# Performance work log

Hardware: AMD Instinct MI355X
Metric: run time of the kernel (lower is better)

The kernel has to match this reference:

```python
import jax, jax.numpy as jnp
import numpy as np

S, D, P, R, E, M, K = 1024, 1024, 2816, 64, 8, 16, 1


def setup_inputs() -> dict:
    key = jax.random.key(0)
    ks = jax.random.split(key, 10)
    xav_a = (2.0 / (P + R)) ** 0.5   # xavier_uniform-like std for adapters
    xav_d = (2.0 / (D + P)) ** 0.5   # xavier for down projections
    bank_s = (1.0 / D) ** 0.5        # keep basis columns O(1)
    return {
        "hidden_states": jax.random.normal(ks[0], (S, D), jnp.float32),
        "expert_indices": jax.random.randint(ks[1], (S, K), 0, E),
        "expert_weights": jax.random.uniform(ks[2], (S, K), jnp.float32),
        "up_adapters": jax.random.normal(ks[3], (E, P, R), jnp.float32) * xav_a,
        "gate_adapters": jax.random.normal(ks[4], (E, P, R), jnp.float32) * xav_a,
        "up_mixture_logits": jax.random.normal(ks[5], (E, M), jnp.float32) * 0.01,
        "gate_mixture_logits": jax.random.normal(ks[6], (E, M), jnp.float32) * 0.01,
        "down_projections": jax.random.normal(ks[7], (E, D, P), jnp.float32) * xav_d,
        "up_bank": jax.random.normal(ks[8], (M, D, R), jnp.float32) * bank_s,
        "gate_bank": jax.random.normal(ks[9], (M, D, R), jnp.float32) * bank_s,
    }


def reference(hidden_states, expert_indices, expert_weights,
              up_adapters, gate_adapters, up_mixture_logits,
              gate_mixture_logits, down_projections, up_bank, gate_bank):
    n_experts = down_projections.shape[0]
    # SparseMixer: token-independent mixture weights over global bases (softmax)
    alpha_up = jax.nn.softmax(up_mixture_logits, axis=-1)      # [E, M]
    alpha_gate = jax.nn.softmax(gate_mixture_logits, axis=-1)  # [E, M]
    # Compose per-expert mixed bases: sum_j alpha_{e,j} B_j -> [E, D, R]
    up_mixed = jnp.einsum('em,mdr->edr', alpha_up, up_bank)
    gate_mixed = jnp.einsum('em,mdr->edr', alpha_gate, gate_bank)
    # Recomposed Up/Gate weights: A_e @ mixed_e^T -> [E, P, D]
    W_up = jnp.einsum('epr,edr->epd', up_adapters, up_mixed)
    W_gate = jnp.einsum('epr,edr->epd', gate_adapters, gate_mixed)
    # Combine routing weights per (token, expert): sum over topk slots
    onehot = (expert_indices[..., None] == jnp.arange(n_experts)).astype(hidden_states.dtype)  # [S,K,E]
    comb = jnp.einsum('ske,sk->se', onehot, expert_weights)  # [S, E]
    out = jnp.zeros_like(hidden_states)
    for e in range(n_experts):  # fixed small expert count
        up = hidden_states @ W_up[e].T        # [S, P]
        gate = hidden_states @ W_gate[e].T    # [S, P]
        inter = jax.nn.silu(gate) * up        # gated activation
        out = out + (inter @ down_projections[e].T) * comb[:, e:e + 1]
    return out
```

## Files before the change

### kernel.cpp

```cpp
#include <hip/hip_runtime.h>
#include <hip/hip_bf16.h>
#include <math.h>

#define S 1024
#define D 1024
#define P 2816
#define R 64
#define E 8
#define M 16
#define KSPLIT 4
#define KQ (P / KSPLIT)
#define NIT (KQ / 64)
#define ZT 16
#define ACH ((E * P * R) / 8)

typedef __attribute__((ext_vector_type(8))) short short8;
typedef __attribute__((ext_vector_type(4))) float floatx4;

static __device__ inline unsigned short f2bf(float f) {
  __hip_bfloat16 h = __float2bfloat16(f);
  return *reinterpret_cast<unsigned short*>(&h);
}
static __device__ inline short8 pack8(float4 a, float4 b) {
  short8 v;
  v[0] = f2bf(a.x); v[1] = f2bf(a.y); v[2] = f2bf(a.z); v[3] = f2bf(a.w);
  v[4] = f2bf(b.x); v[5] = f2bf(b.y); v[6] = f2bf(b.z); v[7] = f2bf(b.w);
  return v;
}

__global__ __launch_bounds__(256) void k_pre(
    const float* __restrict__ H, const float* __restrict__ Aup,
    const float* __restrict__ Agate, const int* __restrict__ idx,
    unsigned short* __restrict__ Hbf, unsigned short* __restrict__ Aubf,
    unsigned short* __restrict__ Agbf, int* __restrict__ perm,
    int* __restrict__ offs) {
  int b = blockIdx.x, t = threadIdx.x;
  int g = b * 256 + t;

  if (b == 0) {
    __shared__ int hist[E];
    __shared__ int basearr[E];
    if (t < E) hist[t] = 0;
    __syncthreads();
    int e4[4];
#pragma unroll
    for (int j = 0; j < 4; ++j) {
      e4[j] = idx[t + j * 256];
      atomicAdd(&hist[e4[j]], 1);
    }
    __syncthreads();
    if (t == 0) {
      int run = 0;
      for (int i = 0; i < E; ++i) { basearr[i] = run; offs[i] = run; run += hist[i]; }
      offs[E] = S;
    }
    __syncthreads();
#pragma unroll
    for (int j = 0; j < 4; ++j) {
      int pos = atomicAdd(&basearr[e4[j]], 1);
      perm[pos] = t + j * 256;
    }
  }

  {
    const float* hs = H + (size_t)g * 16;
    float4 h0 = *(const float4*)hs, h1 = *(const float4*)(hs + 4);
    float4 h2 = *(const float4*)(hs + 8), h3 = *(const float4*)(hs + 12);
    *(short8*)(Hbf + (size_t)g * 16) = pack8(h0, h1);
    *(short8*)(Hbf + (size_t)g * 16 + 8) = pack8(h2, h3);
  }
#pragma unroll
  for (int j = 0; j < 3; ++j) {
    int c = g + j * 65536;
    if (c < ACH) {
      const float* su = Aup + (size_t)c * 8;
      const float* sg = Agate + (size_t)c * 8;
      float4 u0 = *(const float4*)su, u1 = *(const float4*)(su + 4);
      float4 g0 = *(const float4*)sg, g1 = *(const float4*)(sg + 4);
      *(short8*)(Aubf + (size_t)c * 8) = pack8(u0, u1);
      *(short8*)(Agbf + (size_t)c * 8) = pack8(g0, g1);
    }
  }
}

__global__ __launch_bounds__(256) void k_mix(
    const float* __restrict__ up_logits, const float* __restrict__ gate_logits,
    const float* __restrict__ up_bank, const float* __restrict__ gate_bank,
    unsigned short* __restrict__ mxT) {
  int mat = blockIdx.x;
  int d0 = blockIdx.y * 16;
  const float* bank = mat ? gate_bank : up_bank;
  __shared__ float alpha[E][M];
  __shared__ float tile[E][64][17];
  int t = threadIdx.x;
  if (t < E) {
    const float* lg = (mat ? gate_logits : up_logits) + t * M;
    float v[M], mx = -1e30f, s = 0.f;
#pragma unroll
    for (int m = 0; m < M; ++m) { v[m] = lg[m]; mx = fmaxf(mx, v[m]); }
#pragma unroll
    for (int m = 0; m < M; ++m) { v[m] = expf(v[m] - mx); s += v[m]; }
#pragma unroll
    for (int m = 0; m < M; ++m) alpha[t][m] = v[m] / s;
  }
  __syncthreads();
  int r4 = (t & 15) * 4;
  int dg = t >> 4;
  float val[E][4];
#pragma unroll
  for (int e = 0; e < E; ++e)
#pragma unroll
    for (int i = 0; i < 4; ++i) val[e][i] = 0.f;
  for (int m = 0; m < M; ++m) {
    float4 bv = *(const float4*)(bank + ((size_t)m * D + d0 + dg) * R + r4);
#pragma unroll
    for (int e = 0; e < E; ++e) {
      float a = alpha[e][m];
      val[e][0] += a * bv.x; val[e][1] += a * bv.y;
      val[e][2] += a * bv.z; val[e][3] += a * bv.w;
    }
  }
#pragma unroll
  for (int e = 0; e < E; ++e)
#pragma unroll
    for (int i = 0; i < 4; ++i) tile[e][r4 + i][dg] = val[e][i];
  __syncthreads();
  int e = t >> 5;
#pragma unroll
  for (int half = 0; half < 2; ++half) {
    int rr = (t & 31) + half * 32;
    short8 o0, o1;
#pragma unroll
    for (int j = 0; j < 8; ++j) {
      o0[j] = (short)f2bf(tile[e][rr][j]);
      o1[j] = (short)f2bf(tile[e][rr][8 + j]);
    }
    unsigned short* dst = mxT + ((size_t)(e * 128 + mat * 64 + rr)) * D + d0;
    *(short8*)dst = o0;
    *(short8*)(dst + 8) = o1;
  }
}

__global__ __launch_bounds__(64) void k_t(
    const unsigned short* __restrict__ Hbf, const unsigned short* __restrict__ mxT,
    const int* __restrict__ perm, const int* __restrict__ offs,
    float* __restrict__ tpart) {
  int e = blockIdx.x;
  int end = offs[e + 1];
  int row0 = offs[e] + blockIdx.y * 16;
  if (row0 >= end) return;
  int lane = threadIdx.x & 63;
  int quad = lane >> 4, l15 = lane & 15;
  int z = blockIdx.z;
  int k0 = z * (D / ZT);
  int pos = row0 + l15;
  int tok = (pos < end) ? perm[pos] : -1;
  const unsigned short* hrow = Hbf + (size_t)(tok < 0 ? 0 : tok) * D + k0;
  const unsigned short* brow = mxT + (size_t)e * 128 * D + k0;
  floatx4 acc[8];
#pragma unroll
  for (int nt = 0; nt < 8; ++nt) acc[nt] = (floatx4){0.f, 0.f, 0.f, 0.f};
#pragma unroll
  for (int ks = 0; ks < 2; ++ks) {
    int kc = ks * 32 + quad * 8;
    short8 a = (short8){0, 0, 0, 0, 0, 0, 0, 0};
    if (tok >= 0) a = *(const short8*)(hrow + kc);
#pragma unroll
    for (int nt = 0; nt < 8; ++nt) {
      short8 bb = *(const short8*)(brow + (size_t)(nt * 16 + l15) * D + kc);
      acc[nt] = __builtin_amdgcn_mfma_f32_16x16x32_bf16(a, bb, acc[nt], 0, 0, 0);
    }
  }
#pragma unroll
  for (int reg = 0; reg < 4; ++reg) {
    int p = row0 + quad * 4 + reg;
    if (p < end) {
#pragma unroll
      for (int nt = 0; nt < 8; ++nt)
        tpart[((size_t)z * S + p) * 128 + nt * 16 + l15] = acc[nt][reg];
    }
  }
}

__global__ __launch_bounds__(256) void k_tred(
    const float* __restrict__ tpart, unsigned short* __restrict__ tbuf) {
  int i = (blockIdx.x * 256 + threadIdx.x) * 2;
  float2 s = make_float2(0.f, 0.f);
#pragma unroll
  for (int z = 0; z < ZT; ++z) {
    float2 v = *(const float2*)(tpart + (size_t)z * S * 128 + i);
    s.x += v.x; s.y += v.y;
  }
  unsigned int pk = (unsigned int)f2bf(s.x) | ((unsigned int)f2bf(s.y) << 16);
  *(unsigned int*)(tbuf + i) = pk;
}

__global__ __launch_bounds__(256) void k_inter(
    const unsigned short* __restrict__ tbuf, const unsigned short* __restrict__ Aubf,
    const unsigned short* __restrict__ Agbf, const int* __restrict__ offs,
    unsigned short* __restrict__ inter) {
  int e = blockIdx.x;
  int start = offs[e] + blockIdx.y * 16;
  int end = offs[e + 1];
  if (start >= end) return;
  int t = threadIdx.x, lane = t & 63, w = t >> 6;
  int quad = lane >> 4, l15 = lane & 15;
  int p0 = blockIdx.z * 256 + w * 64;
  int pos = start + l15;
  bool okA = pos < end;
  floatx4 accu[4], accg[4];
#pragma unroll
  for (int nt = 0; nt < 4; ++nt) {
    accu[nt] = (floatx4){0.f, 0.f, 0.f, 0.f};
    accg[nt] = (floatx4){0.f, 0.f, 0.f, 0.f};
  }
#pragma unroll
  for (int ks = 0; ks < 2; ++ks) {
    int kc = ks * 32 + quad * 8;
    short8 au = (short8){0, 0, 0, 0, 0, 0, 0, 0};
    short8 ag = (short8){0, 0, 0, 0, 0, 0, 0, 0};
    if (okA) {
      au = *(const short8*)(tbuf + (size_t)pos * 128 + kc);
      ag = *(const short8*)(tbuf + (size_t)pos * 128 + 64 + kc);
    }
#pragma unroll
    for (int nt = 0; nt < 4; ++nt) {
      size_t prow = (size_t)e * P + p0 + nt * 16 + l15;
      short8 bu = *(const short8*)(Aubf + prow * R + kc);
      short8 bg = *(const short8*)(Agbf + prow * R + kc);
      accu[nt] = __builtin_amdgcn_mfma_f32_16x16x32_bf16(au, bu, accu[nt], 0, 0, 0);
      accg[nt] = __builtin_amdgcn_mfma_f32_16x16x32_bf16(ag, bg, accg[nt], 0, 0, 0);
    }
  }
#pragma unroll
  for (int nt = 0; nt < 4; ++nt)
#pragma unroll
    for (int reg = 0; reg < 4; ++reg) {
      int prow = start + quad * 4 + reg;
      if (prow < end) {
        float gv = accg[nt][reg], uv = accu[nt][reg];
        float val = uv * (gv / (1.f + __expf(-gv)));
        inter[(size_t)prow * P + p0 + nt * 16 + l15] = f2bf(val);
      }
    }
}

__global__ __launch_bounds__(256) void k_down(
    const unsigned short* __restrict__ inter, const float* __restrict__ Wd,
    const int* __restrict__ offs, float* __restrict__ dpart) {
  int e = blockIdx.x;
  int start = offs[e];
  int end = offs[e + 1];
  if (start >= end) return;
  int kz = blockIdx.y;
  int d0 = blockIdx.z * 64;
  __shared__ unsigned short As[256][72];
  __shared__ unsigned short Bs[64][72];
  int t = threadIdx.x;
  int lane = t & 63, w = t >> 6, quad = lane >> 4, l15 = lane & 15;

  const unsigned short* aptr[8];
  bool aok[8];
#pragma unroll
  for (int j = 0; j < 8; ++j) {
    int arow = (t >> 3) + 32 * j;
    int pos = start + arow;
    aok[j] = (pos < end);
    aptr[j] = inter + (size_t)(aok[j] ? pos : start) * P + kz * KQ + (t & 7) * 8;
  }
  const float* bsrc = Wd + ((size_t)(e * D + d0 + (t >> 2)) * P + kz * KQ + (t & 3) * 16);

  float4 pa[8];
  float4 pb[4];
#pragma unroll
  for (int j = 0; j < 8; ++j)
    pa[j] = aok[j] ? *(const float4*)(aptr[j]) : make_float4(0.f, 0.f, 0.f, 0.f);
#pragma unroll
  for (int q = 0; q < 4; ++q) pb[q] = *(const float4*)(bsrc + q * 4);

  floatx4 acc[4][4];
#pragma unroll
  for (int tt = 0; tt < 4; ++tt)
#pragma unroll
    for (int dt = 0; dt < 4; ++dt) acc[tt][dt] = (floatx4){0.f, 0.f, 0.f, 0.f};

  for (int it = 0; it < NIT; ++it) {
#pragma unroll
    for (int j = 0; j < 8; ++j)
      *(float4*)&As[(t >> 3) + 32 * j][(t & 7) * 8] = pa[j];
    {
      short8 bv0, bv1;
      bv0[0] = f2bf(pb[0].x); bv0[1] = f2bf(pb[0].y); bv0[2] = f2bf(pb[0].z); bv0[3] = f2bf(pb[0].w);
      bv0[4] = f2bf(pb[1].x); bv0[5] = f2bf(pb[1].y); bv0[6] = f2bf(pb[1].z); bv0[7] = f2bf(pb[1].w);
      bv1[0] = f2bf(pb[2].x); bv1[1] = f2bf(pb[2].y); bv1[2] = f2bf(pb[2].z); bv1[3] = f2bf(pb[2].w);
      bv1[4] = f2bf(pb[3].x); bv1[5] = f2bf(pb[3].y); bv1[6] = f2bf(pb[3].z); bv1[7] = f2bf(pb[3].w);
      *(short8*)&Bs[t >> 2][(t & 3) * 16] = bv0;
      *(short8*)&Bs[t >> 2][(t & 3) * 16 + 8] = bv1;
    }
    __syncthreads();
    if (it + 1 < NIT) {
      int k0 = (it + 1) * 64;
#pragma unroll
      for (int j = 0; j < 8; ++j)
        pa[j] = aok[j] ? *(const float4*)(aptr[j] + k0) : make_float4(0.f, 0.f, 0.f, 0.f);
#pragma unroll
      for (int q = 0; q < 4; ++q) pb[q] = *(const float4*)(bsrc + k0 + q * 4);
    }
#pragma unroll
    for (int ks = 0; ks < 2; ++ks) {
      int kc = ks * 32 + quad * 8;
      short8 a[4], b[4];
#pragma unroll
      for (int tt = 0; tt < 4; ++tt) a[tt] = *(const short8*)&As[w * 64 + tt * 16 + l15][kc];
#pragma unroll
      for (int dt = 0; dt < 4; ++dt) b[dt] = *(const short8*)&Bs[dt * 16 + l15][kc];
#pragma unroll
      for (int tt = 0; tt < 4; ++tt)
#pragma unroll
        for (int dt = 0; dt < 4; ++dt)
          acc[tt][dt] = __builtin_amdgcn_mfma_f32_16x16x32_bf16(a[tt], b[dt], acc[tt][dt], 0, 0, 0);
    }
    __syncthreads();
  }
  float* dp = dpart + (size_t)kz * S * D;
#pragma unroll
  for (int tt = 0; tt < 4; ++tt)
#pragma unroll
    for (int reg = 0; reg < 4; ++reg) {
      int pos = start + w * 64 + tt * 16 + quad * 4 + reg;
      if (pos < end) {
#pragma unroll
        for (int dt = 0; dt < 4; ++dt)
          dp[(size_t)pos * D + d0 + dt * 16 + l15] = acc[tt][dt][reg];
      }
    }
}

__global__ __launch_bounds__(256) void k_red(
    const float* __restrict__ dpart, const int* __restrict__ perm,
    const float* __restrict__ wts, float* __restrict__ out) {
  int t = threadIdx.x;
  int row = blockIdx.x * 4 + (t >> 6);
  int lane = t & 63;
  int tok = perm[row];
  float wt = wts[tok];
  const float* src = dpart + (size_t)row * D + lane * 4;
  float* dst = out + (size_t)tok * D + lane * 4;
#pragma unroll
  for (int j = 0; j < 4; ++j) {
    float4 s = *(const float4*)(src + j * 256);
#pragma unroll
    for (int kz = 1; kz < KSPLIT; ++kz) {
      float4 v = *(const float4*)(src + (size_t)kz * S * D + j * 256);
      s.x += v.x; s.y += v.y; s.z += v.z; s.w += v.w;
    }
    s.x *= wt; s.y *= wt; s.z *= wt; s.w *= wt;
    *(float4*)(dst + j * 256) = s;
  }
}

extern "C" void kernel_launch(void* const* d_in, const int* in_sizes, int n_in,
                              void* d_out, int out_size, void* d_ws, size_t ws_size,
                              hipStream_t stream) {
  const float* H = (const float*)d_in[0];
  const int* idx = (const int*)d_in[1];
  const float* wts = (const float*)d_in[2];
  const float* Aup = (const float*)d_in[3];
  const float* Agate = (const float*)d_in[4];
  const float* upl = (const float*)d_in[5];
  const float* gatel = (const float*)d_in[6];
  const float* Wd = (const float*)d_in[7];
  const float* upb = (const float*)d_in[8];
  const float* gateb = (const float*)d_in[9];
  float* out = (float*)d_out;

  char* ws = (char*)d_ws;
  unsigned short* Hbf = (unsigned short*)ws;
  unsigned short* mxT = Hbf + (size_t)S * D;
  unsigned short* Aubf = mxT + (size_t)E * 128 * D;
  unsigned short* Agbf = Aubf + (size_t)E * P * R;
  unsigned short* inter = Agbf + (size_t)E * P * R;
  unsigned short* tbuf = inter + (size_t)S * P;
  float* tpart = (float*)(tbuf + (size_t)S * 128);
  float* dpart = tpart + (size_t)ZT * S * 128;
  int* perm = (int*)(dpart + (size_t)KSPLIT * S * D);
  int* offs = perm + S;

  k_pre<<<256, 256, 0, stream>>>(H, Aup, Agate, idx, Hbf, Aubf, Agbf, perm, offs);
  k_mix<<<dim3(2, D / 16), 256, 0, stream>>>(upl, gatel, upb, gateb, mxT);
  k_t<<<dim3(E, 16, ZT), 64, 0, stream>>>(Hbf, mxT, perm, offs, tpart);
  k_tred<<<256, 256, 0, stream>>>(tpart, tbuf);
  k_inter<<<dim3(E, 16, P / 256), 256, 0, stream>>>(tbuf, Aubf, Agbf, offs, inter);
  k_down<<<dim3(E, KSPLIT, D / 64), 256, 0, stream>>>(inter, Wd, offs, dpart);
  k_red<<<256, 256, 0, stream>>>(dpart, perm, wts, out);
}
```

Before: 214.9 us.

## Fuse all stages into one persistent kernel with grid-wide barriers

Replaces the seven separate kernel launches with a single 512-block persistent kernel whose phases are separated by atomic-counter grid barriers. The T-projection is reorganised so each block reduces four wave partials in shared memory, which cuts the Z-split from 16 to 4. The tpart reduction is folded into the inter stage, removing the tbuf buffer. This removes launch gaps and intermediate passes, but every phase now runs on a fixed 512 blocks, so the down-projection and other stages may get less parallelism, and the spin barriers depend on all blocks being co-resident.

```diff
diff --git a/kernel.cpp b/kernel.cpp
--- a/kernel.cpp
+++ b/kernel.cpp
@@ -11,8 +11,9 @@
 #define KSPLIT 4
 #define KQ (P / KSPLIT)
 #define NIT (KQ / 64)
-#define ZT 16
+#define ZT 4
 #define ACH ((E * P * R) / 8)
+#define NBLK 512
 
 typedef __attribute__((ext_vector_type(8))) short short8;
 typedef __attribute__((ext_vector_type(4))) float floatx4;
@@ -28,334 +29,330 @@
   return v;
 }
 
-__global__ __launch_bounds__(256) void k_pre(
-    const float* __restrict__ H, const float* __restrict__ Aup,
-    const float* __restrict__ Agate, const int* __restrict__ idx,
-    unsigned short* __restrict__ Hbf, unsigned short* __restrict__ Aubf,
-    unsigned short* __restrict__ Agbf, int* __restrict__ perm,
-    int* __restrict__ offs) {
+static __device__ __forceinline__ void gbar(unsigned* ctr) {
+  __syncthreads();
+  if (threadIdx.x == 0) {
+    __threadfence();
+    __hip_atomic_fetch_add(ctr, 1u, __ATOMIC_RELEASE, __HIP_MEMORY_SCOPE_AGENT);
+    while (__hip_atomic_load(ctr, __ATOMIC_ACQUIRE, __HIP_MEMORY_SCOPE_AGENT) < NBLK)
+      __builtin_amdgcn_s_sleep(4);
+    __threadfence();
+  }
+  __syncthreads();
+}
+
+__global__ __launch_bounds__(256) void k_mega(
+    const float* __restrict__ H, const int* __restrict__ idx,
+    const float* __restrict__ wts, const float* __restrict__ Aup,
+    const float* __restrict__ Agate, const float* __restrict__ upl,
+    const float* __restrict__ gatel, const float* __restrict__ Wd,
+    const float* __restrict__ upb, const float* __restrict__ gateb,
+    unsigned short* __restrict__ Hbf, unsigned short* __restrict__ mxT,
+    unsigned short* __restrict__ Aubf, unsigned short* __restrict__ Agbf,
+    unsigned short* __restrict__ inter, float* __restrict__ tpart,
+    float* __restrict__ dpart, int* __restrict__ perm,
+    int* __restrict__ offs, float* __restrict__ out,
+    unsigned* __restrict__ bars) {
+  __shared__ __align__(16) unsigned char smem[46080];
   int b = blockIdx.x, t = threadIdx.x;
-  int g = b * 256 + t;
-
-  if (b == 0) {
-    __shared__ int hist[E];
-    __shared__ int basearr[E];
-    if (t < E) hist[t] = 0;
+  int lane = t & 63, w = t >> 6, quad = lane >> 4, l15 = lane & 15;
+
+  if (b < 256) {
+    int g = b * 256 + t;
+    if (b == 0) {
+      int* hist = (int*)smem;
+      int* basearr = hist + E;
+      if (t < E) hist[t] = 0;
+      __syncthreads();
+      int e4[4];
+#pragma unroll
+      for (int j = 0; j < 4; ++j) {
+        e4[j] = idx[t + j * 256];
+        atomicAdd(&hist[e4[j]], 1);
+      }
+      __syncthreads();
+      if (t == 0) {
+        int run = 0;
+        for (int i = 0; i < E; ++i) { basearr[i] = run; offs[i] = run; run += hist[i]; }
+        offs[E] = S;
+      }
+      __syncthreads();
+#pragma unroll
+      for (int j = 0; j < 4; ++j) {
+        int pos = atomicAdd(&basearr[e4[j]], 1);
+        perm[pos] = t + j * 256;
+      }
+    }
+    {
+      const float* hs = H + (size_t)g * 16;
+      float4 h0 = *(const float4*)hs, h1 = *(const float4*)(hs + 4);
+      float4 h2 = *(const float4*)(hs + 8), h3 = *(const float4*)(hs + 12);
+      *(short8*)(Hbf + (size_t)g * 16) = pack8(h0, h1);
+      *(short8*)(Hbf + (size_t)g * 16 + 8) = pack8(h2, h3);
+    }
+#pragma unroll
+    for (int j = 0; j < 3; ++j) {
+      int c = g + j * 65536;
+      if (c < ACH) {
+        const float* su = Aup + (size_t)c * 8;
+        const float* sg = Agate + (size_t)c * 8;
+        float4 u0 = *(const float4*)su, u1 = *(const float4*)(su + 4);
+        float4 g0 = *(const float4*)sg, g1 = *(const float4*)(sg + 4);
+        *(short8*)(Aubf + (size_t)c * 8) = pack8(u0, u1);
+        *(short8*)(Agbf + (size_t)c * 8) = pack8(g0, g1);
+      }
+    }
+  } else if (b < 384) {
+    int mb = b - 256;
+    int mat = mb >> 6, d0 = (mb & 63) * 16;
+    const float* bank = mat ? gateb : upb;
+    float* tile = (float*)smem;
+    float* alpha = (float*)(smem + 34816);
+    if (t < E) {
+      const float* lg = (mat ? gatel : upl) + t * M;
+      float v[M], mx = -1e30f, s = 0.f;
+#pragma unroll
+      for (int m = 0; m < M; ++m) { v[m] = lg[m]; mx = fmaxf(mx, v[m]); }
+#pragma unroll
+      for (int m = 0; m < M; ++m) { v[m] = expf(v[m] - mx); s += v[m]; }
+#pragma unroll
+      for (int m = 0; m < M; ++m) alpha[t * M + m] = v[m] / s;
+    }
     __syncthreads();
-    int e4[4];
-#pragma unroll
-    for (int j = 0; j < 4; ++j) {
-      e4[j] = idx[t + j * 256];
-      atomicAdd(&hist[e4[j]], 1);
-    }
+    int r4 = (t & 15) * 4;
+    int dg = t >> 4;
+    float val[E][4];
+#pragma unroll
+    for (int e = 0; e < E; ++e)
+#pragma unroll
+      for (int i = 0; i < 4; ++i) val[e][i] = 0.f;
+    for (int m = 0; m < M; ++m) {
+      float4 bv = *(const float4*)(bank + ((size_t)m * D + d0 + dg) * R + r4);
+#pragma unroll
+      for (int e = 0; e < E; ++e) {
+        float a = alpha[e * M + m];
+        val[e][0] += a * bv.x; val[e][1] += a * bv.y;
+        val[e][2] += a * bv.z; val[e][3] += a * bv.w;
+      }
+    }
+#pragma unroll
+    for (int e = 0; e < E; ++e)
+#pragma unroll
+      for (int i = 0; i < 4; ++i) tile[((size_t)e * 64 + r4 + i) * 17 + dg] = val[e][i];
     __syncthreads();
-    if (t == 0) {
-      int run = 0;
-      for (int i = 0; i < E; ++i) { basearr[i] = run; offs[i] = run; run += hist[i]; }
-      offs[E] = S;
-    }
-    __syncthreads();
-#pragma unroll
-    for (int j = 0; j < 4; ++j) {
-      int pos = atomicAdd(&basearr[e4[j]], 1);
-      perm[pos] = t + j * 256;
-    }
-  }
+    int e = t >> 5;
+#pragma unroll
+    for (int half = 0; half < 2; ++half) {
+      int rr = (t & 31) + half * 32;
+      short8 o0, o1;
+#pragma unroll
+      for (int j = 0; j < 8; ++j) {
+        o0[j] = (short)f2bf(tile[((size_t)e * 64 + rr) * 17 + j]);
+        o1[j] = (short)f2bf(tile[((size_t)e * 64 + rr) * 17 + 8 + j]);
+      }
+      unsigned short* dst = mxT + ((size_t)(e * 128 + mat * 64 + rr)) * D + d0;
+      *(short8*)dst = o0;
+      *(short8*)(dst + 8) = o1;
+    }
+  }
+  gbar(&bars[0]);
 
   {
-    const float* hs = H + (size_t)g * 16;
-    float4 h0 = *(const float4*)hs, h1 = *(const float4*)(hs + 4);
-    float4 h2 = *(const float4*)(hs + 8), h3 = *(const float4*)(hs + 12);
-    *(short8*)(Hbf + (size_t)g * 16) = pack8(h0, h1);
-    *(short8*)(Hbf + (size_t)g * 16 + 8) = pack8(h2, h3);
-  }
-#pragma unroll
-  for (int j = 0; j < 3; ++j) {
-    int c = g + j * 65536;
-    if (c < ACH) {
-      const float* su = Aup + (size_t)c * 8;
-      const float* sg = Agate + (size_t)c * 8;
-      float4 u0 = *(const float4*)su, u1 = *(const float4*)(su + 4);
-      float4 g0 = *(const float4*)sg, g1 = *(const float4*)(sg + 4);
-      *(short8*)(Aubf + (size_t)c * 8) = pack8(u0, u1);
-      *(short8*)(Agbf + (size_t)c * 8) = pack8(g0, g1);
-    }
-  }
-}
-
-__global__ __launch_bounds__(256) void k_mix(
-    const float* __restrict__ up_logits, const float* __restrict__ gate_logits,
-    const float* __restrict__ up_bank, const float* __restrict__ gate_bank,
-    unsigned short* __restrict__ mxT) {
-  int mat = blockIdx.x;
-  int d0 = blockIdx.y * 16;
-  const float* bank = mat ? gate_bank : up_bank;
-  __shared__ float alpha[E][M];
-  __shared__ float tile[E][64][17];
-  int t = threadIdx.x;
-  if (t < E) {
-    const float* lg = (mat ? gate_logits : up_logits) + t * M;
-    float v[M], mx = -1e30f, s = 0.f;
-#pragma unroll
-    for (int m = 0; m < M; ++m) { v[m] = lg[m]; mx = fmaxf(mx, v[m]); }
-#pragma unroll
-    for (int m = 0; m < M; ++m) { v[m] = expf(v[m] - mx); s += v[m]; }
-#pragma unroll
-    for (int m = 0; m < M; ++m) alpha[t][m] = v[m] / s;
-  }
-  __syncthreads();
-  int r4 = (t & 15) * 4;
-  int dg = t >> 4;
-  float val[E][4];
-#pragma unroll
-  for (int e = 0; e < E; ++e)
-#pragma unroll
-    for (int i = 0; i < 4; ++i) val[e][i] = 0.f;
-  for (int m = 0; m < M; ++m) {
-    float4 bv = *(const float4*)(bank + ((size_t)m * D + d0 + dg) * R + r4);
-#pragma unroll
-    for (int e = 0; e < E; ++e) {
-      float a = alpha[e][m];
-      val[e][0] += a * bv.x; val[e][1] += a * bv.y;
-      val[e][2] += a * bv.z; val[e][3] += a * bv.w;
-    }
-  }
-#pragma unroll
-  for (int e = 0; e < E; ++e)
-#pragma unroll
-    for (int i = 0; i < 4; ++i) tile[e][r4 + i][dg] = val[e][i];
-  __syncthreads();
-  int e = t >> 5;
-#pragma unroll
-  for (int half = 0; half < 2; ++half) {
-    int rr = (t & 31) + half * 32;
-    short8 o0, o1;
-#pragma unroll
-    for (int j = 0; j < 8; ++j) {
-      o0[j] = (short)f2bf(tile[e][rr][j]);
-      o1[j] = (short)f2bf(tile[e][rr][8 + j]);
-    }
-    unsigned short* dst = mxT + ((size_t)(e * 128 + mat * 64 + rr)) * D + d0;
-    *(short8*)dst = o0;
-    *(short8*)(dst + 8) = o1;
-  }
-}
-
-__global__ __launch_bounds__(64) void k_t(
-    const unsigned short* __restrict__ Hbf, const unsigned short* __restrict__ mxT,
-    const int* __restrict__ perm, const int* __restrict__ offs,
-    float* __restrict__ tpart) {
-  int e = blockIdx.x;
-  int end = offs[e + 1];
-  int row0 = offs[e] + blockIdx.y * 16;
-  if (row0 >= end) return;
-  int lane = threadIdx.x & 63;
-  int quad = lane >> 4, l15 = lane & 15;
-  int z = blockIdx.z;
-  int k0 = z * (D / ZT);
-  int pos = row0 + l15;
-  int tok = (pos < end) ? perm[pos] : -1;
-  const unsigned short* hrow = Hbf + (size_t)(tok < 0 ? 0 : tok) * D + k0;
-  const unsigned short* brow = mxT + (size_t)e * 128 * D + k0;
-  floatx4 acc[8];
-#pragma unroll
-  for (int nt = 0; nt < 8; ++nt) acc[nt] = (floatx4){0.f, 0.f, 0.f, 0.f};
-#pragma unroll
-  for (int ks = 0; ks < 2; ++ks) {
-    int kc = ks * 32 + quad * 8;
-    short8 a = (short8){0, 0, 0, 0, 0, 0, 0, 0};
-    if (tok >= 0) a = *(const short8*)(hrow + kc);
-#pragma unroll
-    for (int nt = 0; nt < 8; ++nt) {
-      short8 bb = *(const short8*)(brow + (size_t)(nt * 16 + l15) * D + kc);
-      acc[nt] = __builtin_amdgcn_mfma_f32_16x16x32_bf16(a, bb, acc[nt], 0, 0, 0);
-    }
-  }
-#pragma unroll
-  for (int reg = 0; reg < 4; ++reg) {
-    int p = row0 + quad * 4 + reg;
-    if (p < end) {
-#pragma unroll
-      for (int nt = 0; nt < 8; ++nt)
-        tpart[((size_t)z * S + p) * 128 + nt * 16 + l15] = acc[nt][reg];
-    }
-  }
-}
-
-__global__ __launch_bounds__(256) void k_tred(
-    const float* __restrict__ tpart, unsigned short* __restrict__ tbuf) {
-  int i = (blockIdx.x * 256 + threadIdx.x) * 2;
-  float2 s = make_float2(0.f, 0.f);
-#pragma unroll
-  for (int z = 0; z < ZT; ++z) {
-    float2 v = *(const float2*)(tpart + (size_t)z * S * 128 + i);
-    s.x += v.x; s.y += v.y;
-  }
-  unsigned int pk = (unsigned int)f2bf(s.x) | ((unsigned int)f2bf(s.y) << 16);
-  *(unsigned int*)(tbuf + i) = pk;
-}
-
-__global__ __launch_bounds__(256) void k_inter(
-    const unsigned short* __restrict__ tbuf, const unsigned short* __restrict__ Aubf,
-    const unsigned short* __restrict__ Agbf, const int* __restrict__ offs,
-    unsigned short* __restrict__ inter) {
-  int e = blockIdx.x;
-  int start = offs[e] + blockIdx.y * 16;
-  int end = offs[e + 1];
-  if (start >= end) return;
-  int t = threadIdx.x, lane = t & 63, w = t >> 6;
-  int quad = lane >> 4, l15 = lane & 15;
-  int p0 = blockIdx.z * 256 + w * 64;
-  int pos = start + l15;
-  bool okA = pos < end;
-  floatx4 accu[4], accg[4];
-#pragma unroll
-  for (int nt = 0; nt < 4; ++nt) {
-    accu[nt] = (floatx4){0.f, 0.f, 0.f, 0.f};
-    accg[nt] = (floatx4){0.f, 0.f, 0.f, 0.f};
-  }
-#pragma unroll
-  for (int ks = 0; ks < 2; ++ks) {
-    int kc = ks * 32 + quad * 8;
-    short8 au = (short8){0, 0, 0, 0, 0, 0, 0, 0};
-    short8 ag = (short8){0, 0, 0, 0, 0, 0, 0, 0};
-    if (okA) {
-      au = *(const short8*)(tbuf + (size_t)pos * 128 + kc);
-      ag = *(const short8*)(tbuf + (size_t)pos * 128 + 64 + kc);
-    }
-#pragma unroll
-    for (int nt = 0; nt < 4; ++nt) {
-      size_t prow = (size_t)e * P + p0 + nt * 16 + l15;
-      short8 bu = *(const short8*)(Aubf + prow * R + kc);
-      short8 bg = *(const short8*)(Agbf + prow * R + kc);
-      accu[nt] = __builtin_amdgcn_mfma_f32_16x16x32_bf16(au, bu, accu[nt], 0, 0, 0);
-      accg[nt] = __builtin_amdgcn_mfma_f32_16x16x32_bf16(ag, bg, accg[nt], 0, 0, 0);
-    }
-  }
-#pragma unroll
-  for (int nt = 0; nt < 4; ++nt)
-#pragma unroll
-    for (int reg = 0; reg < 4; ++reg) {
-      int prow = start + quad * 4 + reg;
-      if (prow < end) {
-        float gv = accg[nt][reg], uv = accu[nt][reg];
-        float val = uv * (gv / (1.f + __expf(-gv)));
-        inter[(size_t)prow * P + p0 + nt * 16 + l15] = f2bf(val);
-      }
-    }
-}
-
-__global__ __launch_bounds__(256) void k_down(
-    const unsigned short* __restrict__ inter, const float* __restrict__ Wd,
-    const int* __restrict__ offs, float* __restrict__ dpart) {
-  int e = blockIdx.x;
-  int start = offs[e];
-  int end = offs[e + 1];
-  if (start >= end) return;
-  int kz = blockIdx.y;
-  int d0 = blockIdx.z * 64;
-  __shared__ unsigned short As[256][72];
-  __shared__ unsigned short Bs[64][72];
-  int t = threadIdx.x;
-  int lane = t & 63, w = t >> 6, quad = lane >> 4, l15 = lane & 15;
-
-  const unsigned short* aptr[8];
-  bool aok[8];
-#pragma unroll
-  for (int j = 0; j < 8; ++j) {
-    int arow = (t >> 3) + 32 * j;
-    int pos = start + arow;
-    aok[j] = (pos < end);
-    aptr[j] = inter + (size_t)(aok[j] ? pos : start) * P + kz * KQ + (t & 7) * 8;
-  }
-  const float* bsrc = Wd + ((size_t)(e * D + d0 + (t >> 2)) * P + kz * KQ + (t & 3) * 16);
-
-  float4 pa[8];
-  float4 pb[4];
-#pragma unroll
-  for (int j = 0; j < 8; ++j)
-    pa[j] = aok[j] ? *(const float4*)(aptr[j]) : make_float4(0.f, 0.f, 0.f, 0.f);
-#pragma unroll
-  for (int q = 0; q < 4; ++q) pb[q] = *(const float4*)(bsrc + q * 4);
-
-  floatx4 acc[4][4];
-#pragma unroll
-  for (int tt = 0; tt < 4; ++tt)
-#pragma unroll
-    for (int dt = 0; dt < 4; ++dt) acc[tt][dt] = (floatx4){0.f, 0.f, 0.f, 0.f};
-
-  for (int it = 0; it < NIT; ++it) {
-#pragma unroll
-    for (int j = 0; j < 8; ++j)
-      *(float4*)&As[(t >> 3) + 32 * j][(t & 7) * 8] = pa[j];
-    {
-      short8 bv0, bv1;
-      bv0[0] = f2bf(pb[0].x); bv0[1] = f2bf(pb[0].y); bv0[2] = f2bf(pb[0].z); bv0[3] = f2bf(pb[0].w);
-      bv0[4] = f2bf(pb[1].x); bv0[5] = f2bf(pb[1].y); bv0[6] = f2bf(pb[1].z); bv0[7] = f2bf(pb[1].w);
-      bv1[0] = f2bf(pb[2].x); bv1[1] = f2bf(pb[2].y); bv1[2] = f2bf(pb[2].z); bv1[3] = f2bf(pb[2].w);
-      bv1[4] = f2bf(pb[3].x); bv1[5] = f2bf(pb[3].y); bv1[6] = f2bf(pb[3].z); bv1[7] = f2bf(pb[3].w);
-      *(short8*)&Bs[t >> 2][(t & 3) * 16] = bv0;
-      *(short8*)&Bs[t >> 2][(t & 3) * 16 + 8] = bv1;
-    }
-    __syncthreads();
-    if (it + 1 < NIT) {
-      int k0 = (it + 1) * 64;
+    int e = b >> 6, y = (b >> 2) & 15, z = b & 3;
+    int end = offs[e + 1];
+    int row0 = offs[e] + y * 16;
+    if (row0 < end) {
+      int k0 = z * 256 + w * 64;
+      int pos = row0 + l15;
+      int tok = (pos < end) ? perm[pos] : -1;
+      const unsigned short* hrow = Hbf + (size_t)(tok < 0 ? 0 : tok) * D + k0;
+      const unsigned short* brow = mxT + (size_t)e * 128 * D + k0;
+      floatx4 acc[8];
+#pragma unroll
+      for (int nt = 0; nt < 8; ++nt) acc[nt] = (floatx4){0.f, 0.f, 0.f, 0.f};
+#pragma unroll
+      for (int ks = 0; ks < 2; ++ks) {
+        int kc = ks * 32 + quad * 8;
+        short8 a = (short8){0, 0, 0, 0, 0, 0, 0, 0};
+        if (tok >= 0) a = *(const short8*)(hrow + kc);
+#pragma unroll
+        for (int nt = 0; nt < 8; ++nt) {
+          short8 bb = *(const short8*)(brow + (size_t)(nt * 16 + l15) * D + kc);
+          acc[nt] = __builtin_amdgcn_mfma_f32_16x16x32_bf16(a, bb, acc[nt], 0, 0, 0);
+        }
+      }
+      float* part = (float*)smem;
+#pragma unroll
+      for (int reg = 0; reg < 4; ++reg)
+#pragma unroll
+        for (int nt = 0; nt < 8; ++nt)
+          part[w * 2048 + (quad * 4 + reg) * 128 + nt * 16 + l15] = acc[nt][reg];
+      __syncthreads();
+#pragma unroll
+      for (int i = 0; i < 8; ++i) {
+        int el = t * 8 + i;
+        float s = part[el] + part[2048 + el] + part[4096 + el] + part[6144 + el];
+        int rr = el >> 7, nn = el & 127;
+        int p = row0 + rr;
+        if (p < end) tpart[((size_t)z * S + p) * 128 + nn] = s;
+      }
+    }
+  }
+  gbar(&bars[1]);
+
+  {
+    int e = b >> 6, y = (b >> 2) & 15, pz = b & 3;
+    int end = offs[e + 1];
+    int start = offs[e] + y * 16;
+    if (start < end) {
+      unsigned short* tb = (unsigned short*)smem;
+#pragma unroll
+      for (int i = 0; i < 8; ++i) {
+        int el = t * 8 + i;
+        int rr = el >> 7, nn = el & 127;
+        int p = start + rr;
+        float s = 0.f;
+        if (p < end) {
+#pragma unroll
+          for (int z = 0; z < ZT; ++z) s += tpart[((size_t)z * S + p) * 128 + nn];
+        }
+        tb[el] = f2bf(s);
+      }
+      __syncthreads();
+      int pbase = pz * 704 + w * 176;
+      short8 au[2], ag[2];
+#pragma unroll
+      for (int ks = 0; ks < 2; ++ks) {
+        int kc = ks * 32 + quad * 8;
+        au[ks] = *(const short8*)&tb[l15 * 128 + kc];
+        ag[ks] = *(const short8*)&tb[l15 * 128 + 64 + kc];
+      }
+#pragma unroll
+      for (int nt = 0; nt < 11; ++nt) {
+        floatx4 accu = (floatx4){0.f, 0.f, 0.f, 0.f};
+        floatx4 accg = (floatx4){0.f, 0.f, 0.f, 0.f};
+        size_t prow = (size_t)e * P + pbase + nt * 16 + l15;
+#pragma unroll
+        for (int ks = 0; ks < 2; ++ks) {
+          int kc = ks * 32 + quad * 8;
+          short8 bu = *(const short8*)(Aubf + prow * R + kc);
+          short8 bg = *(const short8*)(Agbf + prow * R + kc);
+          accu = __builtin_amdgcn_mfma_f32_16x16x32_bf16(au[ks], bu, accu, 0, 0, 0);
+          accg = __builtin_amdgcn_mfma_f32_16x16x32_bf16(ag[ks], bg, accg, 0, 0, 0);
+        }
+#pragma unroll
+        for (int reg = 0; reg < 4; ++reg) {
+          int pr = start + quad * 4 + reg;
+          if (pr < end) {
+            float gv = accg[reg], uv = accu[reg];
+            float val = uv * (gv / (1.f + __expf(-gv)));
+            inter[(size_t)pr * P + pbase + nt * 16 + l15] = f2bf(val);
+          }
+        }
+      }
+    }
+  }
+  gbar(&bars[2]);
+
+  {
+    int e = b >> 6, kz = (b >> 4) & 3, d0 = (b & 15) * 64;
+    int start = offs[e];
+    int end = offs[e + 1];
+    if (start < end) {
+      unsigned short* As = (unsigned short*)smem;
+      unsigned short* Bs = (unsigned short*)(smem + 36864);
+      const unsigned short* aptr[8];
+      bool aok[8];
+#pragma unroll
+      for (int j = 0; j < 8; ++j) {
+        int arow = (t >> 3) + 32 * j;
+        int pos = start + arow;
+        aok[j] = (pos < end);
+        aptr[j] = inter + (size_t)(aok[j] ? pos : start) * P + kz * KQ + (t & 7) * 8;
+      }
+      const float* bsrc = Wd + ((size_t)(e * D + d0 + (t >> 2)) * P + kz * KQ + (t & 3) * 16);
+
+      float4 pa[8];
+      float4 pb[4];
 #pragma unroll
       for (int j = 0; j < 8; ++j)
-        pa[j] = aok[j] ? *(const float4*)(aptr[j] + k0) : make_float4(0.f, 0.f, 0.f, 0.f);
-#pragma unroll
-      for (int q = 0; q < 4; ++q) pb[q] = *(const float4*)(bsrc + k0 + q * 4);
-    }
-#pragma unroll
-    for (int ks = 0; ks < 2; ++ks) {
-      int kc = ks * 32 + quad * 8;
-      short8 a[4], b[4];
-#pragma unroll
-      for (int tt = 0; tt < 4; ++tt) a[tt] = *(const short8*)&As[w * 64 + tt * 16 + l15][kc];
-#pragma unroll
-      for (int dt = 0; dt < 4; ++dt) b[dt] = *(const short8*)&Bs[dt * 16 + l15][kc];
+        pa[j] = aok[j] ? *(const float4*)(aptr[j]) : make_float4(0.f, 0.f, 0.f, 0.f);
+#pragma unroll
+      for (int q = 0; q < 4; ++q) pb[q] = *(const float4*)(bsrc + q * 4);
+
+      floatx4 acc[4][4];
 #pragma unroll
       for (int tt = 0; tt < 4; ++tt)
 #pragma unroll
-        for (int dt = 0; dt < 4; ++dt)
-          acc[tt][dt] = __builtin_amdgcn_mfma_f32_16x16x32_bf16(a[tt], b[dt], acc[tt][dt], 0, 0, 0);
-    }
-    __syncthreads();
-  }
-  float* dp = dpart + (size_t)kz * S * D;
-#pragma unroll
-  for (int tt = 0; tt < 4; ++tt)
-#pragma unroll
-    for (int reg = 0; reg < 4; ++reg) {
-      int pos = start + w * 64 + tt * 16 + quad * 4 + reg;
-      if (pos < end) {
-#pragma unroll
-        for (int dt = 0; dt < 4; ++dt)
-          dp[(size_t)pos * D + d0 + dt * 16 + l15] = acc[tt][dt][reg];
-      }
-    }
-}
-
-__global__ __launch_bounds__(256) void k_red(
-    const float* __restrict__ dpart, const int* __restrict__ perm,
-    const float* __restrict__ wts, float* __restrict__ out) {
-  int t = threadIdx.x;
-  int row = blockIdx.x * 4 + (t >> 6);
-  int lane = t & 63;
-  int tok = perm[row];
-  float wt = wts[tok];
-  const float* src = dpart + (size_t)row * D + lane * 4;
-  float* dst = out + (size_t)tok * D + lane * 4;
-#pragma unroll
-  for (int j = 0; j < 4; ++j) {
-    float4 s = *(const float4*)(src + j * 256);
-#pragma unroll
-    for (int kz = 1; kz < KSPLIT; ++kz) {
-      float4 v = *(const float4*)(src + (size_t)kz * S * D + j * 256);
-      s.x += v.x; s.y += v.y; s.z += v.z; s.w += v.w;
-    }
-    s.x *= wt; s.y *= wt; s.z *= wt; s.w *= wt;
-    *(float4*)(dst + j * 256) = s;
+        for (int dt = 0; dt < 4; ++dt) acc[tt][dt] = (floatx4){0.f, 0.f, 0.f, 0.f};
+
+      for (int it = 0; it < NIT; ++it) {
+#pragma unroll
+        for (int j = 0; j < 8; ++j)
+          *(float4*)&As[((t >> 3) + 32 * j) * 72 + (t & 7) * 8] = pa[j];
+        *(short8*)&Bs[(t >> 2) * 72 + (t & 3) * 16] = pack8(pb[0], pb[1]);
+        *(short8*)&Bs[(t >> 2) * 72 + (t & 3) * 16 + 8] = pack8(pb[2], pb[3]);
+        __syncthreads();
+        if (it + 1 < NIT) {
+          int k0 = (it + 1) * 64;
+#pragma unroll
+          for (int j = 0; j < 8; ++j)
+            pa[j] = aok[j] ? *(const float4*)(aptr[j] + k0) : make_float4(0.f, 0.f, 0.f, 0.f);
+#pragma unroll
+          for (int q = 0; q < 4; ++q) pb[q] = *(const float4*)(bsrc + k0 + q * 4);
+        }
+#pragma unroll
+        for (int ks = 0; ks < 2; ++ks) {
+          int kc = ks * 32 + quad * 8;
+          short8 a[4], bb[4];
+#pragma unroll
+          for (int tt = 0; tt < 4; ++tt)
+            a[tt] = *(const short8*)&As[(w * 64 + tt * 16 + l15) * 72 + kc];
+#pragma unroll
+          for (int dt = 0; dt < 4; ++dt)
+            bb[dt] = *(const short8*)&Bs[(dt * 16 + l15) * 72 + kc];
+#pragma unroll
+          for (int tt = 0; tt < 4; ++tt)
+#pragma unroll
+            for (int dt = 0; dt < 4; ++dt)
+              acc[tt][dt] = __builtin_amdgcn_mfma_f32_16x16x32_bf16(a[tt], bb[dt], acc[tt][dt], 0, 0, 0);
+        }
+        __syncthreads();
+      }
+      float* dp = dpart + (size_t)kz * S * D;
+#pragma unroll
+      for (int tt = 0; tt < 4; ++tt)
+#pragma unroll
+        for (int reg = 0; reg < 4; ++reg) {
+          int pos = start + w * 64 + tt * 16 + quad * 4 + reg;
+          if (pos < end) {
+#pragma unroll
+            for (int dt = 0; dt < 4; ++dt)
+              dp[(size_t)pos * D + d0 + dt * 16 + l15] = acc[tt][dt][reg];
+          }
+        }
+    }
+  }
+  gbar(&bars[3]);
+
+  {
+    int row = b * 2 + (t >> 7);
+    int l = t & 127;
+    int tok = perm[row];
+    float wt = wts[tok];
+    const float* src = dpart + (size_t)row * D + l * 8;
+    float* dst = out + (size_t)tok * D + l * 8;
+#pragma unroll
+    for (int j = 0; j < 2; ++j) {
+      float4 s = *(const float4*)(src + j * 4);
+#pragma unroll
+      for (int kz = 1; kz < KSPLIT; ++kz) {
+        float4 v = *(const float4*)(src + (size_t)kz * S * D + j * 4);
+        s.x += v.x; s.y += v.y; s.z += v.z; s.w += v.w;
+      }
+      s.x *= wt; s.y *= wt; s.z *= wt; s.w *= wt;
+      *(float4*)(dst + j * 4) = s;
+    }
   }
 }
 
@@ -380,17 +377,14 @@
   unsigned short* Aubf = mxT + (size_t)E * 128 * D;
   unsigned short* Agbf = Aubf + (size_t)E * P * R;
   unsigned short* inter = Agbf + (size_t)E * P * R;
-  unsigned short* tbuf = inter + (size_t)S * P;
-  float* tpart = (float*)(tbuf + (size_t)S * 128);
+  float* tpart = (float*)(inter + (size_t)S * P);
   float* dpart = tpart + (size_t)ZT * S * 128;
   int* perm = (int*)(dpart + (size_t)KSPLIT * S * D);
   int* offs = perm + S;
-
-  k_pre<<<256, 256, 0, stream>>>(H, Aup, Agate, idx, Hbf, Aubf, Agbf, perm, offs);
-  k_mix<<<dim3(2, D / 16), 256, 0, stream>>>(upl, gatel, upb, gateb, mxT);
-  k_t<<<dim3(E, 16, ZT), 64, 0, stream>>>(Hbf, mxT, perm, offs, tpart);
-  k_tred<<<256, 256, 0, stream>>>(tpart, tbuf);
-  k_inter<<<dim3(E, 16, P / 256), 256, 0, stream>>>(tbuf, Aubf, Agbf, offs, inter);
-  k_down<<<dim3(E, KSPLIT, D / 64), 256, 0, stream>>>(inter, Wd, offs, dpart);
-  k_red<<<256, 256, 0, stream>>>(dpart, perm, wts, out);
-}
+  unsigned* bars = (unsigned*)(offs + (E + 1));
+
+  hipMemsetAsync(bars, 0, 4 * sizeof(unsigned), stream);
+  k_mega<<<NBLK, 256, 0, stream>>>(H, idx, wts, Aup, Agate, upl, gatel, Wd,
+                                   upb, gateb, Hbf, mxT, Aubf, Agbf, inter,
+                                   tpart, dpart, perm, offs, out, bars);
+}
```

After: 660.5 us. +207.3%, slower.
